# Performance work log

Hardware: AMD Instinct MI355X
Metric: run time of the kernel (lower is better)

The kernel has to match this reference:

```python
import jax, jax.numpy as jnp
import numpy as np

N_ATOMS = 131072
N_MOLS = 4096
D = 128
N_DEPTH = 128
EPS = 1e-07
MEMBERSHIPS = np.array([(-1.645, 0.283), (-1.08, 0.17), (-0.739, 0.134), (-0.468, 0.118),
                        (-0.228, 0.114), (0.0, 0.114), (0.228, 0.114), (0.468, 0.118),
                        (0.739, 0.134), (1.08, 0.17), (1.645, 0.283)], dtype=np.float32)


def setup_inputs() -> dict:
    key = jax.random.key(0)
    k1, k2, k3, k4 = jax.random.split(key, 4)
    x = jax.random.normal(k1, (N_ATOMS, D), dtype=jnp.float32)
    atom_split = jnp.sort(jax.random.randint(k2, (N_ATOMS,), 0, N_MOLS)).astype(jnp.int64)
    W = jax.random.normal(k3, (D * 11, N_DEPTH), dtype=jnp.float32) * 0.02
    b = jax.random.normal(k4, (N_DEPTH,), dtype=jnp.float32) * 0.02
    return {"x": x, "atom_split": atom_split, "W": W, "b": b}


def reference(x, atom_split, W, b):
    means = jnp.asarray(MEMBERSHIPS[:, 0])          # [11]
    stds = jnp.asarray(MEMBERSHIPS[:, 1])           # [11]
    log_norm = jnp.log(stds * np.sqrt(2.0 * np.pi)) # [11]
    # Normal log_prob: -0.5*((x-m)/s)^2 - log(s*sqrt(2pi)); dist_max = log_prob(m) = -log_norm
    z = (x[:, :, None] - means) / stds              # [N, D, 11]
    logp = -0.5 * z * z - log_norm
    out = logp / (-log_norm)                        # divide by log_prob at mean
    out = (out + EPS) / (jnp.sum(out, axis=2, keepdims=True) + EPS)
    out = out.reshape(-1, D * 11)                   # [N, D*11]
    mols = jax.ops.segment_sum(out, atom_split, num_segments=N_MOLS)  # [M, D*11]
    return jnp.tanh(mols @ W + b)                   # [M, n_depth]
```

## Files before the change

### kernel.cpp

```cpp
#include <hip/hip_runtime.h>
#include <math.h>

#define N_ATOMS 131072
#define N_MOLS  4096
#define DFEAT   128
#define NK      11
#define KDIM3   384
#define N_DEPTH 128
#define EPS_F   1e-7f

__constant__ float c_means[NK] = {-1.645f, -1.08f, -0.739f, -0.468f, -0.228f,
                                  0.0f, 0.228f, 0.468f, 0.739f, 1.08f, 1.645f};
__constant__ float c_stds[NK]  = {0.283f, 0.17f, 0.134f, 0.118f, 0.114f,
                                  0.114f, 0.114f, 0.118f, 0.134f, 0.17f, 0.283f};


__global__ __launch_bounds__(256) void wxform_offsets_kernel(
    const float* __restrict__ W,
    const int*   __restrict__ split,
    float*       __restrict__ Bt,
    int*         __restrict__ offsets) {
  const int bid = blockIdx.x;
  const int tid = threadIdx.x;
  if (bid < 192) {
    int t = bid * 256 + tid;
    int n = t & 127;
    int row = t >> 7;
    int j = row >> 7;
    int d = row & 127;
    float acc = 0.0f;
#pragma unroll
    for (int k = 0; k < NK; ++k) {
      float m = c_means[k], s = c_stds[k];
      float a = 0.5f / (s * s * logf(s * 2.5066282746310002f));
      float coef = (j == 2) ? a
                 : (j == 1) ? (-2.0f * a * m)
                            : fmaf(a, m * m, 1.0f + EPS_F);
      acc = fmaf(coef, W[(size_t)(d * NK + k) * N_DEPTH + n], acc);
    }
    Bt[(size_t)row * N_DEPTH + n] = acc;
  } else {
    int t = (bid - 192) * 256 + tid;
    if (t <= N_MOLS) {
      int lo = 0, hi = N_ATOMS;
      while (lo < hi) { int mid = (lo + hi) >> 1; if (split[mid] < t) lo = mid + 1; else hi = mid; }
      offsets[t] = lo;
    }
  }
}

__global__ __launch_bounds__(256) void memb_sums_kernel(
    const float* __restrict__ x,
    const int*   __restrict__ offsets,
    float*       __restrict__ S) {
  const int m   = blockIdx.x;
  const int tid = threadIdx.x;
  const int fq  = tid & 31;
  const int g   = tid >> 5;

  float C2 = 0.0f, C1 = 0.0f, C0 = 11.0f + EPS_F;
#pragma unroll
  for (int k = 0; k < NK; ++k) {
    float m_ = c_means[k], s_ = c_stds[k];
    float a = 0.5f / (s_ * s_ * logf(s_ * 2.5066282746310002f));
    C2 += a;
    C1 = fmaf(-2.0f * a, m_, C1);
    C0 = fmaf(a, m_ * m_, C0);
  }

  const int start = offsets[m];
  const int end   = offsets[m + 1];

  float Sr[4]   = {0.f, 0.f, 0.f, 0.f};
  float Sxr[4]  = {0.f, 0.f, 0.f, 0.f};
  float Sxxr[4] = {0.f, 0.f, 0.f, 0.f};

  for (int a = start + g; a < end; a += 8) {
    float4 v = *(const float4*)&x[(size_t)a * DFEAT + fq * 4];
    float xv[4] = {v.x, v.y, v.z, v.w};
#pragma unroll
    for (int i = 0; i < 4; ++i) {
      float den = fmaf(fmaf(C2, xv[i], C1), xv[i], C0);
      float r   = __builtin_amdgcn_rcpf(den);
      float u   = xv[i] * r;
      Sr[i]  += r;
      Sxr[i] += u;
      Sxxr[i] = fmaf(xv[i], u, Sxxr[i]);
    }
  }

  __shared__ float red[8][32][13];
#pragma unroll
  for (int i = 0; i < 4; ++i) {
    red[g][fq][i * 3 + 0] = Sr[i];
    red[g][fq][i * 3 + 1] = Sxr[i];
    red[g][fq][i * 3 + 2] = Sxxr[i];
  }
  __syncthreads();

  for (int t = tid; t < KDIM3; t += 256) {
    int j  = t >> 7;
    int f  = t & 127;
    int q  = f >> 2, fi = f & 3;
    float s = 0.0f;
#pragma unroll
    for (int gg = 0; gg < 8; ++gg) s += red[gg][q][fi * 3 + j];
    S[(size_t)m * KDIM3 + t] = s;
  }
}

#define GBM 8

__global__ __launch_bounds__(256) void gemm_bias_tanh_kernel(
    const float* __restrict__ A,
    const float* __restrict__ Bt,
    const float* __restrict__ bias,
    float*       __restrict__ out) {
  __shared__ float As[GBM][KDIM3];
  const int tid = threadIdx.x;
  const int m0  = blockIdx.x * GBM;

#pragma unroll
  for (int i = 0; i < 3; ++i) {
    int idx = i * 256 + tid;
    int r   = idx / 96;
    int kf  = idx % 96;
    *(float4*)&As[r][kf * 4] = *(const float4*)&A[(size_t)(m0 + r) * KDIM3 + kf * 4];
  }
  __syncthreads();

  const int n0 = tid & 63;
  const int g  = tid >> 6;
  const int r0 = 2 * g, r1 = 2 * g + 1;

  float acc00 = 0.f, acc01 = 0.f, acc10 = 0.f, acc11 = 0.f;
#pragma unroll 8
  for (int k = 0; k < KDIM3; ++k) {
    float b0 = Bt[(size_t)k * N_DEPTH + n0];
    float b1 = Bt[(size_t)k * N_DEPTH + n0 + 64];
    float a0 = As[r0][k];
    float a1 = As[r1][k];
    acc00 = fmaf(a0, b0, acc00);
    acc01 = fmaf(a0, b1, acc01);
    acc10 = fmaf(a1, b0, acc10);
    acc11 = fmaf(a1, b1, acc11);
  }

  float bv0 = bias[n0], bv1 = bias[n0 + 64];
  int row0 = m0 + r0, row1 = m0 + r1;
  out[(size_t)row0 * N_DEPTH + n0]      = tanhf(acc00 + bv0);
  out[(size_t)row0 * N_DEPTH + n0 + 64] = tanhf(acc01 + bv1);
  out[(size_t)row1 * N_DEPTH + n0]      = tanhf(acc10 + bv0);
  out[(size_t)row1 * N_DEPTH + n0 + 64] = tanhf(acc11 + bv1);
}

extern "C" void kernel_launch(void* const* d_in, const int* in_sizes, int n_in,
                              void* d_out, int out_size, void* d_ws, size_t ws_size,
                              hipStream_t stream) {
  const float* x     = (const float*)d_in[0];
  const int*   split = (const int*)d_in[1];
  const float* W     = (const float*)d_in[2];
  const float* bias  = (const float*)d_in[3];
  float* out = (float*)d_out;

  float* S       = (float*)d_ws;
  float* Bt      = (float*)((char*)d_ws + (size_t)N_MOLS * KDIM3 * 4);
  int*   offsets = (int*)((char*)Bt + (size_t)KDIM3 * N_DEPTH * 4);

  wxform_offsets_kernel<<<dim3(192 + 17), dim3(256), 0, stream>>>(W, split, Bt, offsets);
  memb_sums_kernel<<<dim3(N_MOLS), dim3(256), 0, stream>>>(x, offsets, S);
  gemm_bias_tanh_kernel<<<dim3(N_MOLS / GBM), dim3(256), 0, stream>>>(S, Bt, bias, out);
}
```

Measured before the change: 123.8 us.

## Fuse per-molecule membership sums with GEMM, bias and tanh into one kernel

Merges the segment-sum kernel and the GEMM kernel so each block reduces 4 molecules into shared memory and then multiplies them directly against the transformed weights. This removes the intermediate S buffer round-trip through global memory and one kernel launch. In exchange, the grid shrinks from 4096 blocks to 1024, each processing molecules serially with extra barriers. The GEMM phase also uses a K-split across two thread halves, which adds a combine step.

Measured after the change: 119.1 us. -3.8%, faster.

```diff
diff --git a/kernel.cpp b/kernel.cpp
--- a/kernel.cpp
+++ b/kernel.cpp
@@ -8,6 +8,7 @@
 #define KDIM3   384
 #define N_DEPTH 128
 #define EPS_F   1e-7f
+#define MPB     4
 
 __constant__ float c_means[NK] = {-1.645f, -1.08f, -0.739f, -0.468f, -0.228f,
                                   0.0f, 0.228f, 0.468f, 0.739f, 1.08f, 1.645f};
@@ -49,14 +50,18 @@
   }
 }
 
-__global__ __launch_bounds__(256) void memb_sums_kernel(
+__global__ __launch_bounds__(256) void fused_sums_gemm_kernel(
     const float* __restrict__ x,
     const int*   __restrict__ offsets,
-    float*       __restrict__ S) {
-  const int m   = blockIdx.x;
+    const float* __restrict__ Bt,
+    const float* __restrict__ bias,
+    float*       __restrict__ out) {
   const int tid = threadIdx.x;
-  const int fq  = tid & 31;
-  const int g   = tid >> 5;
+  const int m0  = blockIdx.x * MPB;
+
+  __shared__ float As[MPB][KDIM3];
+  __shared__ float red[8][32][13];
+  float (*comb)[MPB][DFEAT] = (float (*)[MPB][DFEAT])red;
 
   float C2 = 0.0f, C1 = 0.0f, C0 = 11.0f + EPS_F;
 #pragma unroll
@@ -68,90 +73,85 @@
     C0 = fmaf(a, m_ * m_, C0);
   }
 
-  const int start = offsets[m];
-  const int end   = offsets[m + 1];
+  int offs[MPB + 1];
+#pragma unroll
+  for (int i = 0; i <= MPB; ++i) offs[i] = offsets[m0 + i];
 
-  float Sr[4]   = {0.f, 0.f, 0.f, 0.f};
-  float Sxr[4]  = {0.f, 0.f, 0.f, 0.f};
-  float Sxxr[4] = {0.f, 0.f, 0.f, 0.f};
+  const int fq = tid & 31;
+  const int g  = tid >> 5;
 
-  for (int a = start + g; a < end; a += 8) {
-    float4 v = *(const float4*)&x[(size_t)a * DFEAT + fq * 4];
-    float xv[4] = {v.x, v.y, v.z, v.w};
+  for (int i = 0; i < MPB; ++i) {
+    float Sr[4]   = {0.f, 0.f, 0.f, 0.f};
+    float Sxr[4]  = {0.f, 0.f, 0.f, 0.f};
+    float Sxxr[4] = {0.f, 0.f, 0.f, 0.f};
+
+    for (int a = offs[i] + g; a < offs[i + 1]; a += 8) {
+      float4 v = *(const float4*)&x[(size_t)a * DFEAT + fq * 4];
+      float xv[4] = {v.x, v.y, v.z, v.w};
 #pragma unroll
-    for (int i = 0; i < 4; ++i) {
-      float den = fmaf(fmaf(C2, xv[i], C1), xv[i], C0);
-      float r   = __builtin_amdgcn_rcpf(den);
-      float u   = xv[i] * r;
-      Sr[i]  += r;
-      Sxr[i] += u;
-      Sxxr[i] = fmaf(xv[i], u, Sxxr[i]);
+      for (int q = 0; q < 4; ++q) {
+        float den = fmaf(fmaf(C2, xv[q], C1), xv[q], C0);
+        float r   = __builtin_amdgcn_rcpf(den);
+        float u   = xv[q] * r;
+        Sr[q]  += r;
+        Sxr[q] += u;
+        Sxxr[q] = fmaf(xv[q], u, Sxxr[q]);
+      }
+    }
+
+#pragma unroll
+    for (int q = 0; q < 4; ++q) {
+      red[g][fq][q * 3 + 0] = Sr[q];
+      red[g][fq][q * 3 + 1] = Sxr[q];
+      red[g][fq][q * 3 + 2] = Sxxr[q];
+    }
+    __syncthreads();
+
+    for (int t = tid; t < KDIM3; t += 256) {
+      int j = t >> 7;
+      int f = t & 127;
+      int q = f >> 2, fi = f & 3;
+      float s = 0.0f;
+#pragma unroll
+      for (int gg = 0; gg < 8; ++gg) s += red[gg][q][fi * 3 + j];
+      As[i][t] = s;
+    }
+    __syncthreads();
+  }
+
+  const int n = tid & 127;
+  const int h = tid >> 7;
+  const int kbase = h * (KDIM3 / 2);
+
+  float acc[MPB] = {0.f, 0.f, 0.f, 0.f};
+  for (int kk = 0; kk < KDIM3 / 2; kk += 4) {
+    int k = kbase + kk;
+    float b0 = Bt[(size_t)(k + 0) * N_DEPTH + n];
+    float b1 = Bt[(size_t)(k + 1) * N_DEPTH + n];
+    float b2 = Bt[(size_t)(k + 2) * N_DEPTH + n];
+    float b3 = Bt[(size_t)(k + 3) * N_DEPTH + n];
+#pragma unroll
+    for (int i = 0; i < MPB; ++i) {
+      float4 av = *(const float4*)&As[i][k];
+      acc[i] = fmaf(av.x, b0, acc[i]);
+      acc[i] = fmaf(av.y, b1, acc[i]);
+      acc[i] = fmaf(av.z, b2, acc[i]);
+      acc[i] = fmaf(av.w, b3, acc[i]);
     }
   }
 
-  __shared__ float red[8][32][13];
 #pragma unroll
-  for (int i = 0; i < 4; ++i) {
-    red[g][fq][i * 3 + 0] = Sr[i];
-    red[g][fq][i * 3 + 1] = Sxr[i];
-    red[g][fq][i * 3 + 2] = Sxxr[i];
-  }
+  for (int i = 0; i < MPB; ++i) comb[h][i][n] = acc[i];
   __syncthreads();
 
-  for (int t = tid; t < KDIM3; t += 256) {
-    int j  = t >> 7;
-    int f  = t & 127;
-    int q  = f >> 2, fi = f & 3;
-    float s = 0.0f;
 #pragma unroll
-    for (int gg = 0; gg < 8; ++gg) s += red[gg][q][fi * 3 + j];
-    S[(size_t)m * KDIM3 + t] = s;
+  for (int off = 0; off < (MPB * DFEAT) / 256; ++off) {
+    int idx = off * 256 + tid;
+    int i  = idx >> 7;
+    int nn = idx & 127;
+    float v = comb[0][i][nn] + comb[1][i][nn] + bias[nn];
+    out[(size_t)(m0 + i) * N_DEPTH + nn] = tanhf(v);
   }
-}
-
-#define GBM 8
-
-__global__ __launch_bounds__(256) void gemm_bias_tanh_kernel(
-    const float* __restrict__ A,
-    const float* __restrict__ Bt,
-    const float* __restrict__ bias,
-    float*       __restrict__ out) {
-  __shared__ float As[GBM][KDIM3];
-  const int tid = threadIdx.x;
-  const int m0  = blockIdx.x * GBM;
-
-#pragma unroll
-  for (int i = 0; i < 3; ++i) {
-    int idx = i * 256 + tid;
-    int r   = idx / 96;
-    int kf  = idx % 96;
-    *(float4*)&As[r][kf * 4] = *(const float4*)&A[(size_t)(m0 + r) * KDIM3 + kf * 4];
-  }
-  __syncthreads();
-
-  const int n0 = tid & 63;
-  const int g  = tid >> 6;
-  const int r0 = 2 * g, r1 = 2 * g + 1;
-
-  float acc00 = 0.f, acc01 = 0.f, acc10 = 0.f, acc11 = 0.f;
-#pragma unroll 8
-  for (int k = 0; k < KDIM3; ++k) {
-    float b0 = Bt[(size_t)k * N_DEPTH + n0];
-    float b1 = Bt[(size_t)k * N_DEPTH + n0 + 64];
-    float a0 = As[r0][k];
-    float a1 = As[r1][k];
-    acc00 = fmaf(a0, b0, acc00);
-    acc01 = fmaf(a0, b1, acc01);
-    acc10 = fmaf(a1, b0, acc10);
-    acc11 = fmaf(a1, b1, acc11);
-  }
-
-  float bv0 = bias[n0], bv1 = bias[n0 + 64];
-  int row0 = m0 + r0, row1 = m0 + r1;
-  out[(size_t)row0 * N_DEPTH + n0]      = tanhf(acc00 + bv0);
-  out[(size_t)row0 * N_DEPTH + n0 + 64] = tanhf(acc01 + bv1);
-  out[(size_t)row1 * N_DEPTH + n0]      = tanhf(acc10 + bv0);
-  out[(size_t)row1 * N_DEPTH + n0 + 64] = tanhf(acc11 + bv1);
 }
 
 extern "C" void kernel_launch(void* const* d_in, const int* in_sizes, int n_in,
@@ -163,11 +163,9 @@
   const float* bias  = (const float*)d_in[3];
   float* out = (float*)d_out;
 
-  float* S       = (float*)d_ws;
-  float* Bt      = (float*)((char*)d_ws + (size_t)N_MOLS * KDIM3 * 4);
-  int*   offsets = (int*)((char*)Bt + (size_t)KDIM3 * N_DEPTH * 4);
+  float* Bt      = (float*)d_ws;
+  int*   offsets = (int*)((char*)d_ws + (size_t)KDIM3 * N_DEPTH * 4);
 
   wxform_offsets_kernel<<<dim3(192 + 17), dim3(256), 0, stream>>>(W, split, Bt, offsets);
-  memb_sums_kernel<<<dim3(N_MOLS), dim3(256), 0, stream>>>(x, offsets, S);
-  gemm_bias_tanh_kernel<<<dim3(N_MOLS / GBM), dim3(256), 0, stream>>>(S, Bt, bias, out);
+  fused_sums_gemm_kernel<<<dim3(N_MOLS / MPB), dim3(256), 0, stream>>>(x, offsets, Bt, bias, out);
 }
```
